# Optimization experiments

Hardware: AMD Instinct MI355X
Metric: run time of the kernel (lower is better)

The kernel has to match this reference:

```python
import jax, jax.numpy as jnp
from jax import lax
import numpy as np

# ---- geometry constants (from metadata / module __init__) ----
NA = 1152            # rotview (number of projection angles)
ND = 736             # det_count
NP = 512             # reconstructed image size
VOX = 1.0 / 0.7      # vox_scaling
D   = VOX * 595.0    # source-to-isocenter distance
DD  = VOX * 490.6    # isocenter-to-detector distance
DU  = VOX * 1.2858   # detector pixel spacing
DSD = D + DD         # source-to-detector distance
ANGLES = np.linspace(0.0, 2.0 * np.pi, NA, endpoint=False) + np.pi / 2.0

# ---- Shepp-Logan Fourier filter (skimage/torch-radon construction) ----
PAD = max(64, int(2 ** np.ceil(np.log2(2 * ND))))  # 2048

def _shepp_logan_filter(size):
    n = np.concatenate([np.arange(1, size // 2 + 1, 2),
                        np.arange(size // 2 - 1, 0, -2)])
    f = np.zeros(size)
    f[0] = 0.25
    f[1::2] = -1.0 / (np.pi * n) ** 2
    four = 2.0 * np.real(np.fft.fft(f))            # ramp filter
    omega = np.pi * np.fft.fftfreq(size)[1:]
    four[1:] *= np.sin(omega) / omega              # Shepp-Logan window
    return four[: size // 2 + 1].astype(np.float32)  # rfft half-spectrum

FILT = jnp.asarray(_shepp_logan_filter(PAD))
COS_A = jnp.asarray(np.cos(ANGLES).astype(np.float32))
SIN_A = jnp.asarray(np.sin(ANGLES).astype(np.float32))


def _filter_sinogram(sino):
    # sino: (NA, ND). Zero-pad to PAD, filter in Fourier domain, crop.
    padded = jnp.pad(sino, ((0, 0), (0, PAD - ND)))
    spec = jnp.fft.rfft(padded, axis=-1) * FILT
    filt = jnp.fft.irfft(spec, n=PAD, axis=-1)[:, :ND]
    return filt * (np.pi / (2.0 * NA))


def _backproject(filtered):
    # Pixel-driven fan-beam (flat detector) backprojection.
    c = (NP - 1) / 2.0
    coords = jnp.arange(NP, dtype=jnp.float32) - c
    ys, xs = jnp.meshgrid(coords, coords, indexing='ij')  # (NP, NP)

    def body(acc, inp):
        cb, sb, row = inp
        pdot = xs * cb + ys * sb            # pixel coord along source dir
        pe = -xs * sb + ys * cb             # pixel coord along detector axis
        den = D - pdot                      # source->pixel depth
        u = DSD * pe / den                  # detector coordinate (mm)
        iu = u / DU + (ND - 1) / 2.0        # fractional detector index
        i0 = jnp.floor(iu)
        frac = iu - i0
        i0i = i0.astype(jnp.int32)
        valid = (i0i >= 0) & (i0i < ND - 1) & (den > 0)
        i0c = jnp.clip(i0i, 0, ND - 2)
        v = row[i0c] * (1.0 - frac) + row[i0c + 1] * frac  # linear interp
        w = (D / den) ** 2                   # fan-beam distance weighting
        return acc + jnp.where(valid, w * v, 0.0), None

    img, _ = lax.scan(body, jnp.zeros((NP, NP), jnp.float32),
                      (COS_A, SIN_A, filtered))
    return img


def setup_inputs() -> dict:
    key = jax.random.key(0)
    x = jax.random.normal(key, (1, 1, NA, ND), dtype=jnp.float32)
    return {"x": x}


def reference(x):
    sino = x[0, 0]                          # (NA, ND) after squeeze
    filtered = _filter_sinogram(sino)
    fbp = _backproject(filtered)
    # mu -> HU -> normalize to [0, 1] window
    fbp_hu = (1000.0 * ((fbp - 0.0192) / 0.0192) - (-1024.0)) / (3072.0 - (-1024.0))
    return fbp_hu[None, None]               # (1, 1, 512, 512)
```

## Files before the change

kernel.cpp:

```cpp
#include <hip/hip_runtime.h>
#include <math.h>

#ifndef M_PI
#define M_PI 3.14159265358979323846
#endif

#define NAANG 1152
#define NDET  736
#define NPIX  512
#define PADN  2048
#define NHALF 1025

#define OFF_FILTD 0
#define OFF_H     8320
#define OFF_TRIG  16512
#define OFF_FS    34944
#define OFF_PART  3426432

typedef float f32x2 __attribute__((ext_vector_type(2)));

static __device__ __forceinline__ f32x2 load2(const float* p) {
    f32x2 r;
    __builtin_memcpy(&r, p, 8);
    return r;
}

__global__ void filt_spec_kernel(double* __restrict__ filt_d) {
    __shared__ double red[256];
    const int m = blockIdx.x;
    const int t = threadIdx.x;
    double s = 0.0;
    for (int j = t; j < 1024; j += 256) {
        int n = (j < 512) ? (2 * j + 1) : (2047 - 2 * j);
        double fj = -1.0 / ((M_PI * n) * (M_PI * n));
        double ang = (2.0 * M_PI) * (double)m * (double)(2 * j + 1) / (double)PADN;
        s += fj * cos(ang);
    }
    red[t] = s;
    __syncthreads();
    for (int w = 128; w > 0; w >>= 1) {
        if (t < w) red[t] += red[t + w];
        __syncthreads();
    }
    if (t == 0) {
        double four = 2.0 * (0.25 + red[0]);
        if (m > 0) {
            double om = M_PI * (double)m / (double)PADN;
            four *= sin(om) / om;
        }
        filt_d[m] = four;
    }
}

__global__ void h_kernel(const double* __restrict__ filt_d, float* __restrict__ h,
                         float4* __restrict__ trig) {
    __shared__ double red[256];
    const int k = blockIdx.x;
    const int t = threadIdx.x;
    if (t == 0 && k < NAANG) {
        double ang = 2.0 * M_PI * (double)k / (double)NAANG + M_PI / 2.0;
        double c = cos(ang), s = sin(ang);
        double K = 1085.6 / 1.2858;
        trig[k] = make_float4((float)c, (float)s, (float)(K * c), (float)(K * s));
    }
    double s = 0.0;
    for (int m = t; m <= 1024; m += 256) {
        double c;
        if (m == 0) c = 1.0;
        else if (m == 1024) c = (k & 1) ? -1.0 : 1.0;
        else c = 2.0 * cos((2.0 * M_PI) * (double)m * (double)k / (double)PADN);
        s += filt_d[m] * c;
    }
    red[t] = s;
    __syncthreads();
    for (int w = 128; w > 0; w >>= 1) {
        if (t < w) red[t] += red[t + w];
        __syncthreads();
    }
    if (t == 0)
        h[k] = (float)(red[0] / (double)PADN * (M_PI / (2.0 * (double)NAANG)));
}

__global__ void conv_kernel(const float* __restrict__ x,
                            const float* __restrict__ h,
                            float* __restrict__ fs) {
    __shared__ float sh2[2816];
    __shared__ float srow[NDET];
    const int row = blockIdx.x;
    const int t = threadIdx.x;
    const float4* h4 = (const float4*)h;
    for (int i = t; i < 704; i += 192) ((float4*)sh2)[i] = h4[i & 511];
    const float4* x4 = (const float4*)(x + row * NDET);
    for (int i = t; i < NDET / 4; i += 192) ((float4*)srow)[i] = x4[i];
    __syncthreads();

    const int t4 = 4 * t;
    float o0 = 0.f, o1 = 0.f, o2 = 0.f, o3 = 0.f;
    #pragma unroll 2
    for (int j = 0; j < NDET; j += 4) {
        float4 r4 = *(const float4*)&srow[j];
        const int A = t4 + PADN - j;
        float4 hlo = *(const float4*)&sh2[A - 4];
        float4 hhi = *(const float4*)&sh2[A];
        o0 = fmaf(r4.x, hhi.x, o0); o0 = fmaf(r4.y, hlo.w, o0);
        o0 = fmaf(r4.z, hlo.z, o0); o0 = fmaf(r4.w, hlo.y, o0);
        o1 = fmaf(r4.x, hhi.y, o1); o1 = fmaf(r4.y, hhi.x, o1);
        o1 = fmaf(r4.z, hlo.w, o1); o1 = fmaf(r4.w, hlo.z, o1);
        o2 = fmaf(r4.x, hhi.z, o2); o2 = fmaf(r4.y, hhi.y, o2);
        o2 = fmaf(r4.z, hhi.x, o2); o2 = fmaf(r4.w, hlo.w, o2);
        o3 = fmaf(r4.x, hhi.w, o3); o3 = fmaf(r4.y, hhi.z, o3);
        o3 = fmaf(r4.z, hhi.y, o3); o3 = fmaf(r4.w, hhi.x, o3);
    }
    if (t < NDET / 4)
        *(float4*)&fs[row * NDET + t4] = make_float4(o0, o1, o2, o3);
}

template<int NCH>
__global__ __launch_bounds__(256, 8)
void backproj_kernel(const float* __restrict__ fs,
                     const float4* __restrict__ trig,
                     float* __restrict__ partial) {
    constexpr int ACL = NAANG / NCH;
    __shared__ float4 st[ACL];
    const int t = threadIdx.x;
    const int abase = blockIdx.z * ACL;
    for (int i = t; i < ACL; i += 256) st[i] = trig[abase + i];
    __syncthreads();

    const int ix = blockIdx.x * 256 + t;
    const int iy = blockIdx.y * 4;
    const float xs  = (float)ix - 255.5f;
    const float ys0 = (float)iy - 255.5f;
    const float Dg = 850.0f;

    const float* rowp = fs + (size_t)abase * NDET;
    float acc0 = 0.f, acc1 = 0.f, acc2 = 0.f, acc3 = 0.f;
    for (int a = 0; a < ACL; ++a, rowp += NDET) {
        float4 q = st[a];
        float sb2 = q.y + q.y;
        float kc2 = q.z + q.z;
        float den0 = fmaf(-xs, q.x, fmaf(-ys0, q.y, Dg));
        float kpe0 = fmaf(ys0, q.z, -(xs * q.w));
        float den1 = den0 - q.y, den2 = den0 - sb2, den3 = den2 - q.y;
        float kpe1 = kpe0 + q.z, kpe2 = kpe0 + kc2, kpe3 = kpe2 + q.z;

        float r0 = __builtin_amdgcn_rcpf(den0);
        float r1 = __builtin_amdgcn_rcpf(den1);
        float r2 = __builtin_amdgcn_rcpf(den2);
        float r3 = __builtin_amdgcn_rcpf(den3);
        float iu0 = fmaf(kpe0, r0, 367.5f);
        float iu1 = fmaf(kpe1, r1, 367.5f);
        float iu2 = fmaf(kpe2, r2, 367.5f);
        float iu3 = fmaf(kpe3, r3, 367.5f);
        float f0 = floorf(iu0), f1 = floorf(iu1), f2 = floorf(iu2), f3 = floorf(iu3);
        int   i0 = (int)f0, i1 = (int)f1, i2 = (int)f2, i3 = (int)f3;
        int   c0 = min(max(i0, 0), NDET - 2);
        int   c1 = min(max(i1, 0), NDET - 2);
        int   c2 = min(max(i2, 0), NDET - 2);
        int   c3 = min(max(i3, 0), NDET - 2);
        f32x2 g0 = load2(rowp + c0);
        f32x2 g1 = load2(rowp + c1);
        f32x2 g2 = load2(rowp + c2);
        f32x2 g3 = load2(rowp + c3);
        float fr0 = iu0 - f0, fr1 = iu1 - f1, fr2 = iu2 - f2, fr3 = iu3 - f3;
        float v0 = fmaf(fr0, g0.y - g0.x, g0.x);
        float v1 = fmaf(fr1, g1.y - g1.x, g1.x);
        float v2 = fmaf(fr2, g2.y - g2.x, g2.x);
        float v3 = fmaf(fr3, g3.y - g3.x, g3.x);
        float d0 = Dg * r0, d1 = Dg * r1, d2 = Dg * r2, d3 = Dg * r3;
        float w0 = d0 * d0, w1 = d1 * d1, w2 = d2 * d2, w3 = d3 * d3;
        w0 = ((unsigned)i0 < (unsigned)(NDET - 1)) ? w0 : 0.f;
        w1 = ((unsigned)i1 < (unsigned)(NDET - 1)) ? w1 : 0.f;
        w2 = ((unsigned)i2 < (unsigned)(NDET - 1)) ? w2 : 0.f;
        w3 = ((unsigned)i3 < (unsigned)(NDET - 1)) ? w3 : 0.f;
        acc0 = fmaf(w0, v0, acc0);
        acc1 = fmaf(w1, v1, acc1);
        acc2 = fmaf(w2, v2, acc2);
        acc3 = fmaf(w3, v3, acc3);
    }
    float* outp = partial + ((size_t)blockIdx.z * NPIX + iy) * NPIX + ix;
    outp[0 * NPIX] = acc0;
    outp[1 * NPIX] = acc1;
    outp[2 * NPIX] = acc2;
    outp[3 * NPIX] = acc3;
}

template<int NCH>
__global__ void combine_kernel(const float* __restrict__ partial,
                               float* __restrict__ out) {
    int p = blockIdx.x * 256 + threadIdx.x;
    float s = 0.f;
    #pragma unroll
    for (int c = 0; c < NCH; ++c) s += partial[c * NPIX * NPIX + p];
    out[p] = fmaf(s, (float)(1000.0 / 0.0192 / 4096.0), 0.005859375f);
}

extern "C" void kernel_launch(void* const* d_in, const int* in_sizes, int n_in,
                              void* d_out, int out_size, void* d_ws, size_t ws_size,
                              hipStream_t stream) {
    const float* x = (const float*)d_in[0];
    float* out = (float*)d_out;

    char* ws = (char*)d_ws;
    double* filt_d = (double*)(ws + OFF_FILTD);
    float*  h      = (float*)(ws + OFF_H);
    float4* trig   = (float4*)(ws + OFF_TRIG);
    float*  fs     = (float*)(ws + OFF_FS);
    float*  part   = (float*)(ws + OFF_PART);

    filt_spec_kernel<<<NHALF, 256, 0, stream>>>(filt_d);
    h_kernel<<<PADN, 256, 0, stream>>>(filt_d, h, trig);
    conv_kernel<<<NAANG, 192, 0, stream>>>(x, h, fs);

    const size_t pbytes = (size_t)NPIX * NPIX * 4;
    if (ws_size >= OFF_PART + 8 * pbytes) {
        backproj_kernel<8><<<dim3(2, 128, 8), 256, 0, stream>>>(fs, trig, part);
        combine_kernel<8><<<NPIX * NPIX / 256, 256, 0, stream>>>(part, out);
    } else if (ws_size >= OFF_PART + 4 * pbytes) {
        backproj_kernel<4><<<dim3(2, 128, 4), 256, 0, stream>>>(fs, trig, part);
        combine_kernel<4><<<NPIX * NPIX / 256, 256, 0, stream>>>(part, out);
    } else if (ws_size >= OFF_PART + 2 * pbytes) {
        backproj_kernel<2><<<dim3(2, 128, 2), 256, 0, stream>>>(fs, trig, part);
        combine_kernel<2><<<NPIX * NPIX / 256, 256, 0, stream>>>(part, out);
    } else {
        backproj_kernel<1><<<dim3(2, 128, 1), 256, 0, stream>>>(fs, trig, part);
        combine_kernel<1><<<NPIX * NPIX / 256, 256, 0, stream>>>(part, out);
    }
}
```

Measured before the change: 265.1 us.

## Use float cosine table for filter setup and software-pipeline backprojection loop

Adds a precomputed float cosine table so the filter-spectrum and impulse-response kernels replace per-element double cos calls with table lookups and float accumulation. The backprojection loop is software-pipelined two angles deep: geometry and gathers for the next angle are issued before the previous angle's interpolation is consumed. Trig values are read directly from global memory instead of being staged in LDS. The float reductions may lose some precision relative to the double path, and the pipelining raises register pressure under the 8-waves launch bound.

```diff
diff --git a/kernel.cpp b/kernel.cpp
--- a/kernel.cpp
+++ b/kernel.cpp
@@ -11,11 +11,12 @@
 #define PADN  2048
 #define NHALF 1025
 
-#define OFF_FILTD 0
-#define OFF_H     8320
-#define OFF_TRIG  16512
-#define OFF_FS    34944
-#define OFF_PART  3426432
+#define OFF_COST  0
+#define OFF_FILTF 8192
+#define OFF_H     12416
+#define OFF_TRIG  20608
+#define OFF_FS    39040
+#define OFF_PART  3430528
 
 typedef float f32x2 __attribute__((ext_vector_type(2)));
 
@@ -25,16 +26,21 @@
     return r;
 }
 
-__global__ void filt_spec_kernel(double* __restrict__ filt_d) {
-    __shared__ double red[256];
+__global__ void costab_kernel(float* __restrict__ cosT) {
+    int r = blockIdx.x * 256 + threadIdx.x;
+    cosT[r] = (float)cos(2.0 * M_PI * (double)r / (double)PADN);
+}
+
+__global__ void filt_spec_kernel(const float* __restrict__ cosT,
+                                 float* __restrict__ filt_f) {
+    __shared__ float red[256];
     const int m = blockIdx.x;
     const int t = threadIdx.x;
-    double s = 0.0;
+    float s = 0.f;
     for (int j = t; j < 1024; j += 256) {
         int n = (j < 512) ? (2 * j + 1) : (2047 - 2 * j);
-        double fj = -1.0 / ((M_PI * n) * (M_PI * n));
-        double ang = (2.0 * M_PI) * (double)m * (double)(2 * j + 1) / (double)PADN;
-        s += fj * cos(ang);
+        float fj = (float)(-1.0 / ((M_PI * n) * (M_PI * n)));
+        s += fj * cosT[(m * (2 * j + 1)) & (PADN - 1)];
     }
     red[t] = s;
     __syncthreads();
@@ -43,18 +49,19 @@
         __syncthreads();
     }
     if (t == 0) {
-        double four = 2.0 * (0.25 + red[0]);
+        double four = 2.0 * (0.25 + (double)red[0]);
         if (m > 0) {
             double om = M_PI * (double)m / (double)PADN;
             four *= sin(om) / om;
         }
-        filt_d[m] = four;
-    }
-}
-
-__global__ void h_kernel(const double* __restrict__ filt_d, float* __restrict__ h,
-                         float4* __restrict__ trig) {
-    __shared__ double red[256];
+        filt_f[m] = (float)four;
+    }
+}
+
+__global__ void h_kernel(const float* __restrict__ cosT,
+                         const float* __restrict__ filt_f,
+                         float* __restrict__ h, float4* __restrict__ trig) {
+    __shared__ float red[256];
     const int k = blockIdx.x;
     const int t = threadIdx.x;
     if (t == 0 && k < NAANG) {
@@ -63,13 +70,14 @@
         double K = 1085.6 / 1.2858;
         trig[k] = make_float4((float)c, (float)s, (float)(K * c), (float)(K * s));
     }
-    double s = 0.0;
+    float s = 0.f;
     for (int m = t; m <= 1024; m += 256) {
-        double c;
-        if (m == 0) c = 1.0;
-        else if (m == 1024) c = (k & 1) ? -1.0 : 1.0;
-        else c = 2.0 * cos((2.0 * M_PI) * (double)m * (double)k / (double)PADN);
-        s += filt_d[m] * c;
+        float F = filt_f[m];
+        float c;
+        if (m == 0) c = 1.f;
+        else if (m == 1024) c = (k & 1) ? -1.f : 1.f;
+        else c = 2.f * cosT[(m * k) & (PADN - 1)];
+        s += F * c;
     }
     red[t] = s;
     __syncthreads();
@@ -78,7 +86,7 @@
         __syncthreads();
     }
     if (t == 0)
-        h[k] = (float)(red[0] / (double)PADN * (M_PI / (2.0 * (double)NAANG)));
+        h[k] = (float)((double)red[0] / (double)PADN * (M_PI / (2.0 * (double)NAANG)));
 }
 
 __global__ void conv_kernel(const float* __restrict__ x,
@@ -115,69 +123,81 @@
         *(float4*)&fs[row * NDET + t4] = make_float4(o0, o1, o2, o3);
 }
 
+#define GEO(AA, G0,G1,G2,G3, FR0,FR1,FR2,FR3, W0,W1,W2,W3)               \
+  {                                                                      \
+    float4 q = trig[abase + (AA)];           \
+    float den0 = fmaf(-xs, q.x, fmaf(-ys0, q.y, Dg));                    \
+    float kpe0 = fmaf(ys0, q.z, -(xs * q.w));                            \
+    float sb2 = q.y + q.y, kc2 = q.z + q.z;                              \
+    float den1 = den0 - q.y, den2 = den0 - sb2, den3 = den2 - q.y;       \
+    float kpe1 = kpe0 + q.z, kpe2 = kpe0 + kc2, kpe3 = kpe2 + q.z;       \
+    float r0 = __builtin_amdgcn_rcpf(den0);                              \
+    float r1 = __builtin_amdgcn_rcpf(den1);                              \
+    float r2 = __builtin_amdgcn_rcpf(den2);                              \
+    float r3 = __builtin_amdgcn_rcpf(den3);                              \
+    float iu0 = fmaf(kpe0, r0, 367.5f);                                  \
+    float iu1 = fmaf(kpe1, r1, 367.5f);                                  \
+    float iu2 = fmaf(kpe2, r2, 367.5f);                                  \
+    float iu3 = fmaf(kpe3, r3, 367.5f);                                  \
+    float f0 = floorf(iu0), f1 = floorf(iu1);                            \
+    float f2 = floorf(iu2), f3 = floorf(iu3);                            \
+    int i0 = (int)f0, i1 = (int)f1, i2 = (int)f2, i3 = (int)f3;          \
+    int c0 = min(max(i0, 0), NDET - 2);                                  \
+    int c1 = min(max(i1, 0), NDET - 2);                                  \
+    int c2 = min(max(i2, 0), NDET - 2);                                  \
+    int c3 = min(max(i3, 0), NDET - 2);                                  \
+    const float* rp = fs + (size_t)(abase + (AA)) * NDET;                \
+    G0 = load2(rp + c0); G1 = load2(rp + c1);                            \
+    G2 = load2(rp + c2); G3 = load2(rp + c3);                            \
+    FR0 = iu0 - f0; FR1 = iu1 - f1; FR2 = iu2 - f2; FR3 = iu3 - f3;      \
+    float d0 = Dg * r0, d1 = Dg * r1, d2 = Dg * r2, d3 = Dg * r3;        \
+    W0 = ((unsigned)i0 < (unsigned)(NDET - 1)) ? d0 * d0 : 0.f;          \
+    W1 = ((unsigned)i1 < (unsigned)(NDET - 1)) ? d1 * d1 : 0.f;          \
+    W2 = ((unsigned)i2 < (unsigned)(NDET - 1)) ? d2 * d2 : 0.f;          \
+    W3 = ((unsigned)i3 < (unsigned)(NDET - 1)) ? d3 * d3 : 0.f;          \
+  }
+
+#define CONSUME(G0,G1,G2,G3, FR0,FR1,FR2,FR3, W0,W1,W2,W3)               \
+  {                                                                      \
+    float v0 = fmaf(FR0, G0.y - G0.x, G0.x);                             \
+    float v1 = fmaf(FR1, G1.y - G1.x, G1.x);                             \
+    float v2 = fmaf(FR2, G2.y - G2.x, G2.x);                             \
+    float v3 = fmaf(FR3, G3.y - G3.x, G3.x);                             \
+    acc0 = fmaf(W0, v0, acc0); acc1 = fmaf(W1, v1, acc1);                \
+    acc2 = fmaf(W2, v2, acc2); acc3 = fmaf(W3, v3, acc3);                \
+  }
+
 template<int NCH>
 __global__ __launch_bounds__(256, 8)
 void backproj_kernel(const float* __restrict__ fs,
                      const float4* __restrict__ trig,
                      float* __restrict__ partial) {
     constexpr int ACL = NAANG / NCH;
-    __shared__ float4 st[ACL];
     const int t = threadIdx.x;
     const int abase = blockIdx.z * ACL;
-    for (int i = t; i < ACL; i += 256) st[i] = trig[abase + i];
-    __syncthreads();
-
     const int ix = blockIdx.x * 256 + t;
     const int iy = blockIdx.y * 4;
     const float xs  = (float)ix - 255.5f;
     const float ys0 = (float)iy - 255.5f;
     const float Dg = 850.0f;
 
-    const float* rowp = fs + (size_t)abase * NDET;
     float acc0 = 0.f, acc1 = 0.f, acc2 = 0.f, acc3 = 0.f;
-    for (int a = 0; a < ACL; ++a, rowp += NDET) {
-        float4 q = st[a];
-        float sb2 = q.y + q.y;
-        float kc2 = q.z + q.z;
-        float den0 = fmaf(-xs, q.x, fmaf(-ys0, q.y, Dg));
-        float kpe0 = fmaf(ys0, q.z, -(xs * q.w));
-        float den1 = den0 - q.y, den2 = den0 - sb2, den3 = den2 - q.y;
-        float kpe1 = kpe0 + q.z, kpe2 = kpe0 + kc2, kpe3 = kpe2 + q.z;
-
-        float r0 = __builtin_amdgcn_rcpf(den0);
-        float r1 = __builtin_amdgcn_rcpf(den1);
-        float r2 = __builtin_amdgcn_rcpf(den2);
-        float r3 = __builtin_amdgcn_rcpf(den3);
-        float iu0 = fmaf(kpe0, r0, 367.5f);
-        float iu1 = fmaf(kpe1, r1, 367.5f);
-        float iu2 = fmaf(kpe2, r2, 367.5f);
-        float iu3 = fmaf(kpe3, r3, 367.5f);
-        float f0 = floorf(iu0), f1 = floorf(iu1), f2 = floorf(iu2), f3 = floorf(iu3);
-        int   i0 = (int)f0, i1 = (int)f1, i2 = (int)f2, i3 = (int)f3;
-        int   c0 = min(max(i0, 0), NDET - 2);
-        int   c1 = min(max(i1, 0), NDET - 2);
-        int   c2 = min(max(i2, 0), NDET - 2);
-        int   c3 = min(max(i3, 0), NDET - 2);
-        f32x2 g0 = load2(rowp + c0);
-        f32x2 g1 = load2(rowp + c1);
-        f32x2 g2 = load2(rowp + c2);
-        f32x2 g3 = load2(rowp + c3);
-        float fr0 = iu0 - f0, fr1 = iu1 - f1, fr2 = iu2 - f2, fr3 = iu3 - f3;
-        float v0 = fmaf(fr0, g0.y - g0.x, g0.x);
-        float v1 = fmaf(fr1, g1.y - g1.x, g1.x);
-        float v2 = fmaf(fr2, g2.y - g2.x, g2.x);
-        float v3 = fmaf(fr3, g3.y - g3.x, g3.x);
-        float d0 = Dg * r0, d1 = Dg * r1, d2 = Dg * r2, d3 = Dg * r3;
-        float w0 = d0 * d0, w1 = d1 * d1, w2 = d2 * d2, w3 = d3 * d3;
-        w0 = ((unsigned)i0 < (unsigned)(NDET - 1)) ? w0 : 0.f;
-        w1 = ((unsigned)i1 < (unsigned)(NDET - 1)) ? w1 : 0.f;
-        w2 = ((unsigned)i2 < (unsigned)(NDET - 1)) ? w2 : 0.f;
-        w3 = ((unsigned)i3 < (unsigned)(NDET - 1)) ? w3 : 0.f;
-        acc0 = fmaf(w0, v0, acc0);
-        acc1 = fmaf(w1, v1, acc1);
-        acc2 = fmaf(w2, v2, acc2);
-        acc3 = fmaf(w3, v3, acc3);
-    }
+    f32x2 Ag0, Ag1, Ag2, Ag3, Bg0, Bg1, Bg2, Bg3;
+    float Af0, Af1, Af2, Af3, Aw0, Aw1, Aw2, Aw3;
+    float Bf0, Bf1, Bf2, Bf3, Bw0, Bw1, Bw2, Bw3;
+
+    GEO(0, Ag0,Ag1,Ag2,Ag3, Af0,Af1,Af2,Af3, Aw0,Aw1,Aw2,Aw3);
+    int a = 0;
+    for (; a + 2 < ACL; a += 2) {
+        GEO(a + 1, Bg0,Bg1,Bg2,Bg3, Bf0,Bf1,Bf2,Bf3, Bw0,Bw1,Bw2,Bw3);
+        CONSUME(Ag0,Ag1,Ag2,Ag3, Af0,Af1,Af2,Af3, Aw0,Aw1,Aw2,Aw3);
+        GEO(a + 2, Ag0,Ag1,Ag2,Ag3, Af0,Af1,Af2,Af3, Aw0,Aw1,Aw2,Aw3);
+        CONSUME(Bg0,Bg1,Bg2,Bg3, Bf0,Bf1,Bf2,Bf3, Bw0,Bw1,Bw2,Bw3);
+    }
+    GEO(ACL - 1, Bg0,Bg1,Bg2,Bg3, Bf0,Bf1,Bf2,Bf3, Bw0,Bw1,Bw2,Bw3);
+    CONSUME(Ag0,Ag1,Ag2,Ag3, Af0,Af1,Af2,Af3, Aw0,Aw1,Aw2,Aw3);
+    CONSUME(Bg0,Bg1,Bg2,Bg3, Bf0,Bf1,Bf2,Bf3, Bw0,Bw1,Bw2,Bw3);
+
     float* outp = partial + ((size_t)blockIdx.z * NPIX + iy) * NPIX + ix;
     outp[0 * NPIX] = acc0;
     outp[1 * NPIX] = acc1;
@@ -202,14 +222,16 @@
     float* out = (float*)d_out;
 
     char* ws = (char*)d_ws;
-    double* filt_d = (double*)(ws + OFF_FILTD);
+    float*  cosT   = (float*)(ws + OFF_COST);
+    float*  filt_f = (float*)(ws + OFF_FILTF);
     float*  h      = (float*)(ws + OFF_H);
     float4* trig   = (float4*)(ws + OFF_TRIG);
     float*  fs     = (float*)(ws + OFF_FS);
     float*  part   = (float*)(ws + OFF_PART);
 
-    filt_spec_kernel<<<NHALF, 256, 0, stream>>>(filt_d);
-    h_kernel<<<PADN, 256, 0, stream>>>(filt_d, h, trig);
+    costab_kernel<<<PADN / 256, 256, 0, stream>>>(cosT);
+    filt_spec_kernel<<<NHALF, 256, 0, stream>>>(cosT, filt_f);
+    h_kernel<<<PADN, 256, 0, stream>>>(cosT, filt_f, h, trig);
     conv_kernel<<<NAANG, 192, 0, stream>>>(x, h, fs);
 
     const size_t pbytes = (size_t)NPIX * NPIX * 4;
```

Result: no change. 264.3 us (-0.3%).
